# Kernel tuning notes

Measured on AMD Instinct MI355X. Metric: run time of the kernel, lower is better.

The kernel has to match this reference:

```python
import jax, jax.numpy as jnp
import numpy as np

N_LAYERS, HEADS, D_IN, D_OUT, T, D, DFF = 4, 8, 16, 3, 1024, 512, 2048
D_HEAD = D // HEADS


def sinusoidal_pos_enc(t, d):
    # Faithful to the source: base = pos / 10000**(emb_idx/d); sin on even cols, cos on odd cols
    pos = jnp.arange(t, dtype=jnp.float32)[:, None]
    emb = jnp.arange(d, dtype=jnp.float32)[None, :]
    base = pos / jnp.power(10000.0, emb / d)
    even = (jnp.arange(d) % 2 == 0)[None, :]
    return jnp.where(even, jnp.sin(base), jnp.cos(base))  # (t, d)


def layer_norm(x, g, b, eps=1e-5):
    m = x.mean(-1, keepdims=True)
    v = ((x - m) ** 2).mean(-1, keepdims=True)
    return (x - m) / jnp.sqrt(v + eps) * g + b


def setup_inputs() -> dict:
    key = jax.random.key(0)
    ks = iter(jax.random.split(key, 24))
    s = 0.02
    inp = {}
    inp['x'] = jax.random.normal(next(ks), (16, T, D_IN), dtype=jnp.float32)
    inp['pad_mask'] = jax.random.randint(next(ks), (16, T), 0, 2, dtype=jnp.int32)
    inp['enc_W'] = jax.random.normal(next(ks), (D_IN, D), dtype=jnp.float32) * s
    inp['enc_b'] = jnp.zeros((D,), jnp.float32)
    for name in ['Wq', 'Wk', 'Wv', 'Wo']:
        inp[name] = jax.random.normal(next(ks), (N_LAYERS, D, D), dtype=jnp.float32) * s
    inp['ff_W1'] = jax.random.normal(next(ks), (N_LAYERS, D, DFF), dtype=jnp.float32) * s
    inp['ff_b1'] = jnp.zeros((N_LAYERS, DFF), jnp.float32)
    inp['ff_W2'] = jax.random.normal(next(ks), (N_LAYERS, DFF, D), dtype=jnp.float32) * s
    inp['ff_b2'] = jnp.zeros((N_LAYERS, D), jnp.float32)
    inp['ln1_g'] = jnp.ones((N_LAYERS, D), jnp.float32)
    inp['ln1_b'] = jnp.zeros((N_LAYERS, D), jnp.float32)
    inp['ln2_g'] = jnp.ones((N_LAYERS, D), jnp.float32)
    inp['ln2_b'] = jnp.zeros((N_LAYERS, D), jnp.float32)
    inp['out_W'] = jax.random.normal(next(ks), (D * T, D_OUT), dtype=jnp.float32) * s
    inp['out_b'] = jnp.zeros((D_OUT,), jnp.float32)
    return inp


def reference(x, enc_W, enc_b, Wq, Wk, Wv, Wo, ff_W1, ff_b1, ff_W2, ff_b2,
              ln1_g, ln1_b, ln2_g, ln2_b, out_W, out_b, pad_mask):
    n, t = x.shape[0], x.shape[1]
    # InputEncoding (linear) scaled by sqrt(d_model)
    h = (x @ enc_W + enc_b) * jnp.sqrt(jnp.float32(D))
    # Sinusoidal positional encoding, zeroed at masked (pad_mask==0) timesteps
    pe = sinusoidal_pos_enc(t, D)[None]  # (1, t, d)
    pe = jnp.where(pad_mask[..., None] == 0, 0.0, pe)  # (n, t, d)
    h = h + pe
    mask4 = (pad_mask[..., None, None] == 0)  # (n, t, 1, 1)
    for i in range(N_LAYERS):
        # --- MultiHeadAttention (faithful to source's transpose quirk) ---
        Qh = (h @ Wq[i]).reshape(n, t, HEADS, D_HEAD).swapaxes(2, 3)  # (n,t,dh,H)
        Kh = (h @ Wk[i]).reshape(n, t, HEADS, D_HEAD)                 # (n,t,H,dh)
        Vh = (h @ Wv[i]).reshape(n, t, HEADS, D_HEAD).swapaxes(2, 3)  # (n,t,dh,H)
        # energy: per-timestep (dh x dh), scaled by d_head**1/2 == d_head/2 (source precedence)
        energy = jnp.matmul(Qh, Kh) / (D_HEAD / 2.0)                  # (n,t,dh,dh)
        energy = jnp.where(mask4, -1e20, energy)
        attn = jax.nn.softmax(energy, axis=-1)
        head = jnp.matmul(attn, Vh)                                   # (n,t,dh,H)
        out = head.reshape(n, t, D) @ Wo[i]
        # residual + layer norm
        h = layer_norm(out + h, ln1_g[i], ln1_b[i])
        # --- FFN (relu) ---
        ff = jax.nn.relu(h @ ff_W1[i] + ff_b1[i]) @ ff_W2[i] + ff_b2[i]
        h = layer_norm(ff + h, ln2_g[i], ln2_b[i])
    # mode='train': flatten and project
    return h.reshape(n, -1) @ out_W + out_b  # (n, d_output)
```

## Files before the change

### kernel.cpp

```cpp
#include <hip/hip_runtime.h>
#include <cmath>

#define NB 16
#define TSEQ 1024
#define DIN 16
#define DM 512
#define DFFN 2048
#define NLAYERS 4
#define DOUTN 3
#define ROWS (NB*TSEQ)

typedef unsigned short u16;
typedef unsigned int   u32;
typedef short bf16x8 __attribute__((ext_vector_type(8)));
typedef u16   u16x4  __attribute__((ext_vector_type(4)));
typedef float f32x4  __attribute__((ext_vector_type(4)));

__device__ __forceinline__ float b2f(u16 v) { return __uint_as_float((unsigned)v << 16); }
__device__ __forceinline__ u16 f2b(float f) {
    unsigned u = __float_as_uint(f);
    return (u16)((u + 0x7FFFu + ((u >> 16) & 1u)) >> 16);
}

#define GLL(gp, lp) __builtin_amdgcn_global_load_lds( \
    (const __attribute__((address_space(1))) unsigned int*)(gp), \
    (__attribute__((address_space(3))) unsigned int*)(lp), 16, 0, 0)

template<int PERM>
__global__ __launch_bounds__(256) void transpose_cast(
    const float* __restrict__ in, u16* __restrict__ out,
    int K, int N, size_t in_lstride, size_t out_lstride)
{
    in  += (size_t)blockIdx.z * in_lstride;
    out += (size_t)blockIdx.z * out_lstride;
    __shared__ float t[32][33];
    int bk = blockIdx.x * 32, bn = blockIdx.y * 32;
    int x = threadIdx.x & 31, y = threadIdx.x >> 5;
    #pragma unroll
    for (int i = 0; i < 32; i += 8)
        t[y + i][x] = in[(size_t)(bk + y + i) * N + bn + x];
    __syncthreads();
    #pragma unroll
    for (int i = 0; i < 32; i += 8) {
        int row = bn + y + i;
        if (PERM) row = ((row & 63) << 3) | ((row >> 6) & 7);
        out[(size_t)row * K + bk + x] = f2b(t[x][y + i]);
    }
}

__global__ __launch_bounds__(128) void pe_table_kernel(float* __restrict__ pe)
{
    int t = blockIdx.x;
    int c = threadIdx.x * 4;
    f32x4 o;
    #pragma unroll
    for (int j = 0; j < 4; ++j) {
        int d = c + j;
        float base = (float)t * powf(10000.0f, -(float)d * (1.0f/512.0f));
        o[j] = ((d & 1) == 0) ? sinf(base) : cosf(base);
    }
    *(f32x4*)&pe[(size_t)t * DM + c] = o;
}

__global__ __launch_bounds__(128) void encode_kernel(
    const float* __restrict__ x, const int* __restrict__ pad,
    const float* __restrict__ W, const float* __restrict__ b,
    const float* __restrict__ pe, u16* __restrict__ h)
{
    int row = blockIdx.x;
    int t   = row & (TSEQ - 1);
    int c   = threadIdx.x * 4;
    float acc[4];
    #pragma unroll
    for (int j = 0; j < 4; ++j) acc[j] = b[c + j];
    const float* xr = x + (size_t)row * DIN;
    #pragma unroll
    for (int k = 0; k < DIN; ++k) {
        float xv = xr[k];
        const float* wr = W + (size_t)k * DM + c;
        #pragma unroll
        for (int j = 0; j < 4; ++j) acc[j] += xv * wr[j];
    }
    const float s = 22.62741699796952f;
    bool has_pe = (pad[row] != 0);
    f32x4 pv = *(const f32x4*)&pe[(size_t)t * DM + c];
    u16x4 o;
    #pragma unroll
    for (int j = 0; j < 4; ++j) {
        acc[j] *= s;
        if (has_pe) acc[j] += pv[j];
        o[j] = f2b(acc[j]);
    }
    *(u16x4*)&h[(size_t)row * DM + c] = o;
}

template<int BIAS, int RELU>
__global__ __launch_bounds__(512, 4) void gemm_bf16(
    const u16* __restrict__ A, const u16* __restrict__ Bt,
    const float* __restrict__ bias, u16* __restrict__ C,
    int M, int N, int K)
{
    __shared__ u16 S[4][8192];
    const int tid  = threadIdx.x;
    const int lane = tid & 63;
    const int wid  = tid >> 6;
    const int wr   = wid >> 2;
    const int wc   = wid & 3;

    const int NY  = N >> 7;
    const int nwg = gridDim.x;
    const int cpx = nwg >> 3;
    const int bid = blockIdx.x;
    const int swz = (bid & 7) * cpx + (bid >> 3);
    const int bm  = (swz / NY) * 128;
    const int bn  = (swz % NY) * 128;

    const int srow8 = lane >> 3;
    const int sslot = lane & 7;
    const int scol  = ((sslot ^ srow8) * 8);
    const u16* Ag = A  + (size_t)(bm + wid * 16 + srow8) * K + scol;
    const u16* Bg = Bt + (size_t)(bn + wid * 16 + srow8) * K + scol;

    f32x4 acc[4][2];
    #pragma unroll
    for (int m = 0; m < 4; ++m)
        #pragma unroll
        for (int n = 0; n < 2; ++n)
            acc[m][n] = (f32x4){0.f, 0.f, 0.f, 0.f};

    const int fr  = lane & 15;
    const int grp = lane >> 4;

    auto STAGE = [&](int k0, int d) {
        u16* Al = S[d * 2 + 0] + wid * 1024;
        u16* Bl = S[d * 2 + 1] + wid * 1024;
        #pragma unroll
        for (int i = 0; i < 2; ++i) {
            GLL(Ag + (size_t)(i * 8) * K + k0, Al + i * 512);
            GLL(Bg + (size_t)(i * 8) * K + k0, Bl + i * 512);
        }
    };

    STAGE(0, 0);
    __syncthreads();

    int cur = 0;
    for (int k0 = 0; k0 < K; k0 += 64) {
        if (k0 + 64 < K) STAGE(k0 + 64, cur ^ 1);
        const u16* As = S[cur * 2 + 0];
        const u16* Bs = S[cur * 2 + 1];
        bf16x8 a[4][2];
        #pragma unroll
        for (int m = 0; m < 4; ++m) {
            int row = wr * 64 + m * 16 + fr;
            #pragma unroll
            for (int ks = 0; ks < 2; ++ks) {
                int slot = (ks * 4 + grp) ^ (row & 7);
                a[m][ks] = *(const bf16x8*)(As + row * 64 + slot * 8);
            }
        }
        #pragma unroll
        for (int n = 0; n < 2; ++n) {
            bf16x8 b[2];
            int row = wc * 32 + n * 16 + fr;
            #pragma unroll
            for (int ks = 0; ks < 2; ++ks) {
                int slot = (ks * 4 + grp) ^ (row & 7);
                b[ks] = *(const bf16x8*)(Bs + row * 64 + slot * 8);
            }
            #pragma unroll
            for (int m = 0; m < 4; ++m) {
                acc[m][n] = __builtin_amdgcn_mfma_f32_16x16x32_bf16(a[m][0], b[0], acc[m][n], 0, 0, 0);
                acc[m][n] = __builtin_amdgcn_mfma_f32_16x16x32_bf16(a[m][1], b[1], acc[m][n], 0, 0, 0);
            }
        }
        __syncthreads();
        cur ^= 1;
    }

    float bb[2] = {0.f, 0.f};
    if (BIAS) {
        #pragma unroll
        for (int n = 0; n < 2; ++n) bb[n] = bias[bn + wc * 32 + n * 16 + fr];
    }
    u16* Cs = (u16*)S;
    #pragma unroll
    for (int m = 0; m < 4; ++m)
        #pragma unroll
        for (int n = 0; n < 2; ++n)
            #pragma unroll
            for (int j = 0; j < 4; ++j) {
                int r = wr * 64 + m * 16 + grp * 4 + j;
                int c = wc * 32 + n * 16 + fr;
                float v = acc[m][n][j];
                if (BIAS) v += bb[n];
                if (RELU) v = fmaxf(v, 0.f);
                Cs[r * 136 + c] = f2b(v);
            }
    __syncthreads();
    #pragma unroll
    for (int p = 0; p < 4; ++p) {
        int r = p * 32 + (tid >> 4);
        int c = (tid & 15) * 8;
        bf16x8 v = *(const bf16x8*)(Cs + r * 136 + c);
        *(bf16x8*)(C + (size_t)(bm + r) * N + bn + c) = v;
    }
}

__global__ __launch_bounds__(256) void attn_mfma(
    const u16* __restrict__ QKV, const int* __restrict__ pad,
    u16* __restrict__ O)
{
    constexpr int WLDS = 2560;
    __shared__ u16 sh[4 * WLDS];
    const int wid  = threadIdx.x >> 6;
    const int lane = threadIdx.x & 63;
    const int site = blockIdx.x * 4 + wid;
    u16* P2 = sh + wid * WLDS;
    u16* Ol = P2 + 2048;

    const u16* base = QKV + (size_t)site * 1536;
    const int fr  = lane & 15;
    const int grp = lane >> 4;
    const bf16x8 zb = {0,0,0,0,0,0,0,0};
    const f32x4  zf = {0.f,0.f,0.f,0.f};

    if (pad[site] == 0) {
        bf16x8 vv = *(const bf16x8*)(base + 1024 + lane * 8);
        float s = 0.f;
        #pragma unroll
        for (int j = 0; j < 8; ++j) s += b2f((u16)vv[j]);
        s += __shfl_xor(s, 1); s += __shfl_xor(s, 2); s += __shfl_xor(s, 4);
        s *= (1.0f / 64.0f);
        bf16x8 ov;
        #pragma unroll
        for (int h2 = 0; h2 < 8; ++h2) ov[h2] = (short)f2b(__shfl(s, h2 * 8));
        *(bf16x8*)(O + (size_t)site * DM + lane * 8) = ov;
        return;
    }

    bf16x8 kt[4];
    #pragma unroll
    for (int n = 0; n < 4; ++n)
        kt[n] = (grp == 0) ? *(const bf16x8*)(base + 512 + (n * 16 + fr) * 8) : zb;
    bf16x8 bv[2];
    #pragma unroll
    for (int ks = 0; ks < 2; ++ks)
        bv[ks] = (fr < 8) ? *(const bf16x8*)(base + 1024 + fr * 64 + ks * 32 + grp * 8) : zb;

    const int swz = (fr & 3) ^ (fr >> 2);
    u16x4 pk23[4][2];

    #pragma unroll
    for (int m = 0; m < 4; ++m) {
        bf16x8 aq = (grp == 0) ? *(const bf16x8*)(base + (m * 16 + fr) * 8) : zb;
        f32x4 ev[4];
        #pragma unroll
        for (int n = 0; n < 4; ++n)
            ev[n] = __builtin_amdgcn_mfma_f32_16x16x32_bf16(kt[n], aq, zf, 0, 0, 0);
        f32x4 t0, t1;
        #pragma unroll
        for (int j = 0; j < 4; ++j) { t0[j] = fmaxf(ev[0][j], ev[1][j]); t1[j] = fmaxf(ev[2][j], ev[3][j]); }
        float mx = -1e30f;
        #pragma unroll
        for (int j = 0; j < 4; ++j) mx = fmaxf(mx, fmaxf(t0[j], t1[j]));
        mx = fmaxf(mx, __shfl_xor(mx, 16));
        mx = fmaxf(mx, __shfl_xor(mx, 32));
        float p[4][4];
        float s = 0.f;
        #pragma unroll
        for (int n = 0; n < 4; ++n)
            #pragma unroll
            for (int j = 0; j < 4; ++j) {
                p[n][j] = __expf((ev[n][j] - mx) * 0.03125f);
                s += p[n][j];
            }
        s += __shfl_xor(s, 16);
        s += __shfl_xor(s, 32);
        float inv = 1.0f / s;
        u16x4 pk[4];
        #pragma unroll
        for (int n = 0; n < 4; ++n)
            #pragma unroll
            for (int j = 0; j < 4; ++j) pk[n][j] = f2b(p[n][j] * inv);
        int row = m * 16 + fr;
        #pragma unroll
        for (int n = 0; n < 2; ++n) {
            int chunk = (n * 2 + (grp >> 1)) ^ swz;
            *(u16x4*)(P2 + row * 32 + chunk * 8 + (grp & 1) * 4) = pk[n];
        }
        pk23[m][0] = pk[2];
        pk23[m][1] = pk[3];
    }

    f32x4 pv[4];
    #pragma unroll
    for (int m = 0; m < 4; ++m) {
        int row = m * 16 + fr;
        bf16x8 ap = *(const bf16x8*)(P2 + row * 32 + ((grp ^ swz) * 8));
        pv[m] = __builtin_amdgcn_mfma_f32_16x16x32_bf16(ap, bv[0], zf, 0, 0, 0);
    }
    asm volatile("s_waitcnt lgkmcnt(0)" ::: "memory");
    __builtin_amdgcn_sched_barrier(0);

    #pragma unroll
    for (int m = 0; m < 4; ++m) {
        int row = m * 16 + fr;
        #pragma unroll
        for (int n = 0; n < 2; ++n) {
            int chunk = (n * 2 + (grp >> 1)) ^ swz;
            *(u16x4*)(P2 + row * 32 + chunk * 8 + (grp & 1) * 4) = pk23[m][n];
        }
    }
    #pragma unroll
    for (int m = 0; m < 4; ++m) {
        int row = m * 16 + fr;
        bf16x8 ap = *(const bf16x8*)(P2 + row * 32 + ((grp ^ swz) * 8));
        pv[m] = __builtin_amdgcn_mfma_f32_16x16x32_bf16(ap, bv[1], pv[m], 0, 0, 0);
    }

    #pragma unroll
    for (int m = 0; m < 4; ++m)
        #pragma unroll
        for (int j = 0; j < 4; ++j) {
            int row = m * 16 + grp * 4 + j;
            if (fr < 8) Ol[row * 8 + fr] = f2b(pv[m][j]);
        }
    bf16x8 o = *(const bf16x8*)(Ol + lane * 8);
    *(bf16x8*)(O + (size_t)site * DM + lane * 8) = o;
}

__global__ __launch_bounds__(256) void add_ln_kernel(
    const u16* __restrict__ A, u16* __restrict__ H,
    const float* __restrict__ g, const float* __restrict__ b)
{
    int row  = blockIdx.x * 4 + (threadIdx.x >> 6);
    int lane = threadIdx.x & 63;
    const u16* a = A + (size_t)row * DM + lane * 8;
    u16* h = H + (size_t)row * DM + lane * 8;
    bf16x8 av = *(const bf16x8*)a;
    bf16x8 hv = *(const bf16x8*)h;
    float v[8];
    float s = 0.f;
    #pragma unroll
    for (int j = 0; j < 8; ++j) { v[j] = b2f((u16)av[j]) + b2f((u16)hv[j]); s += v[j]; }
    #pragma unroll
    for (int off = 32; off > 0; off >>= 1) s += __shfl_xor(s, off, 64);
    float mean = s * (1.0f / 512.0f);
    float var = 0.f;
    #pragma unroll
    for (int j = 0; j < 8; ++j) { float d = v[j] - mean; var += d * d; }
    #pragma unroll
    for (int off = 32; off > 0; off >>= 1) var += __shfl_xor(var, off, 64);
    float rstd = rsqrtf(var * (1.0f / 512.0f) + 1e-5f);
    bf16x8 ov;
    #pragma unroll
    for (int j = 0; j < 8; ++j) {
        int d = lane * 8 + j;
        ov[j] = (short)f2b((v[j] - mean) * rstd * g[d] + b[d]);
    }
    *(bf16x8*)h = ov;
}

__global__ __launch_bounds__(256) void out_stage1(
    const u16* __restrict__ h, const float* __restrict__ W,
    float* __restrict__ partial)
{
    int b = blockIdx.x, s = blockIdx.y;
    int tid = threadIdx.x;
    const u16* hb = h + (size_t)b * (TSEQ * DM) + (size_t)s * 8192;
    const float* Wb = W + (size_t)s * 8192 * 3;
    float a0 = 0.f, a1 = 0.f, a2 = 0.f;
    #pragma unroll 4
    for (int it = 0; it < 32; ++it) {
        int i = it * 256 + tid;
        float hv = b2f(hb[i]);
        a0 += hv * Wb[i * 3 + 0];
        a1 += hv * Wb[i * 3 + 1];
        a2 += hv * Wb[i * 3 + 2];
    }
    __shared__ float red[3][256];
    red[0][tid] = a0; red[1][tid] = a1; red[2][tid] = a2;
    __syncthreads();
    for (int off = 128; off > 0; off >>= 1) {
        if (tid < off) {
            red[0][tid] += red[0][tid + off];
            red[1][tid] += red[1][tid + off];
            red[2][tid] += red[2][tid + off];
        }
        __syncthreads();
    }
    if (tid == 0) {
        partial[(b * 64 + s) * 3 + 0] = red[0][0];
        partial[(b * 64 + s) * 3 + 1] = red[1][0];
        partial[(b * 64 + s) * 3 + 2] = red[2][0];
    }
}

__global__ __launch_bounds__(64) void out_stage2(
    const float* __restrict__ partial, const float* __restrict__ ob,
    float* __restrict__ out)
{
    int t = threadIdx.x;
    if (t < NB * DOUTN) {
        int b = t / 3, o = t % 3;
        float s = ob[o];
        for (int k = 0; k < 64; ++k) s += partial[(b * 64 + k) * 3 + o];
        out[t] = s;
    }
}

extern "C" void kernel_launch(void* const* d_in, const int* in_sizes, int n_in,
                              void* d_out, int out_size, void* d_ws, size_t ws_size,
                              hipStream_t stream)
{
    const float* x    = (const float*)d_in[0];
    const int*   pad  = (const int*)  d_in[1];
    const float* encW = (const float*)d_in[2];
    const float* encB = (const float*)d_in[3];
    const float* Wq   = (const float*)d_in[4];
    const float* Wk   = (const float*)d_in[5];
    const float* Wv   = (const float*)d_in[6];
    const float* Wo   = (const float*)d_in[7];
    const float* fW1  = (const float*)d_in[8];
    const float* fb1  = (const float*)d_in[9];
    const float* fW2  = (const float*)d_in[10];
    const float* fb2  = (const float*)d_in[11];
    const float* l1g  = (const float*)d_in[12];
    const float* l1b  = (const float*)d_in[13];
    const float* l2g  = (const float*)d_in[14];
    const float* l2b  = (const float*)d_in[15];
    const float* outW = (const float*)d_in[16];
    const float* outB = (const float*)d_in[17];
    float* out = (float*)d_out;

    const size_t WL  = 3145728;
    const size_t BUF = (size_t)ROWS * DM;
    const size_t need = (4 * WL + 6 * BUF) * sizeof(u16) + (size_t)TSEQ * DM * sizeof(float);
    if (ws_size < need) return;
    u16* wt = (u16*)d_ws;
    u16* h  = wt + 4 * WL;
    u16* b0 = h  + BUF;
    u16* b3 = b0 + 3 * BUF;
    u16* b4 = b3 + BUF;
    float* pe = (float*)(b4 + BUF);

    transpose_cast<1><<<dim3(16,16,4), 256, 0, stream>>>(Wq,  wt + 0,       512,  512,  (size_t)512*512,  WL);
    transpose_cast<1><<<dim3(16,16,4), 256, 0, stream>>>(Wk,  wt + 262144,  512,  512,  (size_t)512*512,  WL);
    transpose_cast<0><<<dim3(16,16,4), 256, 0, stream>>>(Wv,  wt + 524288,  512,  512,  (size_t)512*512,  WL);
    transpose_cast<0><<<dim3(16,16,4), 256, 0, stream>>>(Wo,  wt + 786432,  512,  512,  (size_t)512*512,  WL);
    transpose_cast<0><<<dim3(16,64,4), 256, 0, stream>>>(fW1, wt + 1048576, 512,  2048, (size_t)512*2048, WL);
    transpose_cast<0><<<dim3(64,16,4), 256, 0, stream>>>(fW2, wt + 2097152, 2048, 512,  (size_t)2048*512, WL);

    pe_table_kernel<<<TSEQ, 128, 0, stream>>>(pe);
    encode_kernel<<<ROWS, 128, 0, stream>>>(x, pad, encW, encB, pe, h);

    for (int l = 0; l < NLAYERS; ++l) {
        u16* wl = wt + (size_t)l * WL;
        gemm_bf16<0,0><<<dim3((ROWS/128)*(1536/128)), 512, 0, stream>>>(h, wl, nullptr, b0, ROWS, 1536, DM);
        attn_mfma<<<ROWS/4, 256, 0, stream>>>(b0, pad, b3);
        gemm_bf16<0,0><<<dim3((ROWS/128)*(DM/128)), 512, 0, stream>>>(b3, wl + 786432, nullptr, b4, ROWS, DM, DM);
        add_ln_kernel<<<ROWS/4, 256, 0, stream>>>(b4, h, l1g + l*DM, l1b + l*DM);
        gemm_bf16<1,1><<<dim3((ROWS/128)*(DFFN/128)), 512, 0, stream>>>(h, wl + 1048576, fb1 + (size_t)l*DFFN, b0, ROWS, DFFN, DM);
        gemm_bf16<1,0><<<dim3((ROWS/128)*(DM/128)), 512, 0, stream>>>(b0, wl + 2097152, fb2 + (size_t)l*DM, b4, ROWS, DM, DFFN);
        add_ln_kernel<<<ROWS/4, 256, 0, stream>>>(b4, h, l2g + l*DM, l2b + l*DM);
    }

    out_stage1<<<dim3(NB, 64), 256, 0, stream>>>(h, outW, (float*)b0);
    out_stage2<<<1, 64, 0, stream>>>((float*)b0, outB, out);
}
```

Before: 727.3 us.

## Fuse residual add and LayerNorm into full-row GEMM epilogue for Wo and FFN2

```diff
diff --git a/kernel.cpp b/kernel.cpp
--- a/kernel.cpp
+++ b/kernel.cpp
@@ -207,6 +207,140 @@
     }
 }
 
+template<int BIAS>
+__global__ __launch_bounds__(512, 4) void gemm_ln(
+    const u16* __restrict__ A, const u16* __restrict__ Bt,
+    const float* __restrict__ bias, u16* __restrict__ H,
+    const float* __restrict__ g, const float* __restrict__ b, int K)
+{
+    __shared__ u16 S[2][17408];
+    const int tid  = threadIdx.x;
+    const int lane = tid & 63;
+    const int wid  = tid >> 6;
+
+    const int nwg = gridDim.x;
+    const int cpx = nwg >> 3;
+    const int bid = blockIdx.x;
+    const int swz = (bid & 7) * cpx + (bid >> 3);
+    const int bm  = swz * 32;
+
+    const int arow = (wid & 1) * 16 + (lane >> 2);
+    const int achk = (lane & 3) ^ ((arow >> 1) & 3);
+    const u16* Ag = A + (size_t)(bm + arow) * K + achk * 8;
+    const u16* Bg[4];
+    #pragma unroll
+    for (int j = 0; j < 4; ++j) {
+        int rB = wid * 64 + j * 16 + (lane >> 2);
+        int bchk = (lane & 3) ^ ((rB >> 1) & 3);
+        Bg[j] = Bt + (size_t)rB * K + bchk * 8;
+    }
+
+    f32x4 acc[2][4];
+    #pragma unroll
+    for (int m = 0; m < 2; ++m)
+        #pragma unroll
+        for (int n = 0; n < 4; ++n)
+            acc[m][n] = (f32x4){0.f, 0.f, 0.f, 0.f};
+
+    const int fr  = lane & 15;
+    const int grp = lane >> 4;
+
+    auto STAGE = [&](int k0, int d) {
+        if (wid < 2) GLL(Ag + k0, &S[d][0] + (wid * 64 + lane) * 8);
+        #pragma unroll
+        for (int j = 0; j < 4; ++j)
+            GLL(Bg[j] + k0, &S[d][1024] + ((wid * 4 + j) * 64 + lane) * 8);
+    };
+
+    STAGE(0, 0);
+    __syncthreads();
+
+    int cur = 0;
+    for (int k0 = 0; k0 < K; k0 += 32) {
+        if (k0 + 32 < K) STAGE(k0 + 32, cur ^ 1);
+        const u16* As = &S[cur][0];
+        const u16* Bs = &S[cur][1024];
+        bf16x8 a[2], bfr[4];
+        #pragma unroll
+        for (int m = 0; m < 2; ++m) {
+            int row = m * 16 + fr;
+            int slot = grp ^ ((row >> 1) & 3);
+            a[m] = *(const bf16x8*)(As + row * 32 + slot * 8);
+        }
+        #pragma unroll
+        for (int n = 0; n < 4; ++n) {
+            int row = wid * 64 + n * 16 + fr;
+            int slot = grp ^ ((row >> 1) & 3);
+            bfr[n] = *(const bf16x8*)(Bs + row * 32 + slot * 8);
+        }
+        #pragma unroll
+        for (int n = 0; n < 4; ++n)
+            #pragma unroll
+            for (int m = 0; m < 2; ++m)
+                acc[m][n] = __builtin_amdgcn_mfma_f32_16x16x32_bf16(a[m], bfr[n], acc[m][n], 0, 0, 0);
+        __syncthreads();
+        cur ^= 1;
+    }
+
+    float bb[4] = {0.f, 0.f, 0.f, 0.f};
+    if (BIAS) {
+        #pragma unroll
+        for (int n = 0; n < 4; ++n) bb[n] = bias[wid * 64 + n * 16 + fr];
+    }
+    u16* Cs = &S[0][0];
+    float* gl = (float*)(Cs + 16704);
+    float* bl = gl + 512;
+    #pragma unroll
+    for (int m = 0; m < 2; ++m)
+        #pragma unroll
+        for (int n = 0; n < 4; ++n)
+            #pragma unroll
+            for (int j = 0; j < 4; ++j) {
+                int r = m * 16 + grp * 4 + j;
+                int c = wid * 64 + n * 16 + fr;
+                Cs[r * 520 + c] = f2b(acc[m][n][j] + bb[n]);
+            }
+    gl[tid] = g[tid];
+    bl[tid] = b[tid];
+    __syncthreads();
+
+    int r  = wid * 4 + (lane >> 4);
+    int c0 = (lane & 15) * 32;
+    const u16* cr = Cs + r * 520 + c0;
+    u16* hr = H + (size_t)(bm + r) * DM + c0;
+    float v[32];
+    float s = 0.f;
+    #pragma unroll
+    for (int q = 0; q < 4; ++q) {
+        bf16x8 cv = *(const bf16x8*)(cr + q * 8);
+        bf16x8 hv = *(const bf16x8*)(hr + q * 8);
+        #pragma unroll
+        for (int j = 0; j < 8; ++j) {
+            v[q * 8 + j] = b2f((u16)cv[j]) + b2f((u16)hv[j]);
+            s += v[q * 8 + j];
+        }
+    }
+    s += __shfl_xor(s, 1); s += __shfl_xor(s, 2);
+    s += __shfl_xor(s, 4); s += __shfl_xor(s, 8);
+    float mean = s * (1.0f / 512.0f);
+    float var = 0.f;
+    #pragma unroll
+    for (int q = 0; q < 32; ++q) { float d = v[q] - mean; var += d * d; }
+    var += __shfl_xor(var, 1); var += __shfl_xor(var, 2);
+    var += __shfl_xor(var, 4); var += __shfl_xor(var, 8);
+    float rstd = rsqrtf(var * (1.0f / 512.0f) + 1e-5f);
+    #pragma unroll
+    for (int q = 0; q < 4; ++q) {
+        bf16x8 ov;
+        #pragma unroll
+        for (int j = 0; j < 8; ++j) {
+            int d = c0 + q * 8 + j;
+            ov[j] = (short)f2b((v[q * 8 + j] - mean) * rstd * gl[d] + bl[d]);
+        }
+        *(bf16x8*)(hr + q * 8) = ov;
+    }
+}
+
 __global__ __launch_bounds__(256) void attn_mfma(
     const u16* __restrict__ QKV, const int* __restrict__ pad,
     u16* __restrict__ O)
@@ -328,38 +462,6 @@
         }
     bf16x8 o = *(const bf16x8*)(Ol + lane * 8);
     *(bf16x8*)(O + (size_t)site * DM + lane * 8) = o;
-}
-
-__global__ __launch_bounds__(256) void add_ln_kernel(
-    const u16* __restrict__ A, u16* __restrict__ H,
-    const float* __restrict__ g, const float* __restrict__ b)
-{
-    int row  = blockIdx.x * 4 + (threadIdx.x >> 6);
-    int lane = threadIdx.x & 63;
-    const u16* a = A + (size_t)row * DM + lane * 8;
-    u16* h = H + (size_t)row * DM + lane * 8;
-    bf16x8 av = *(const bf16x8*)a;
-    bf16x8 hv = *(const bf16x8*)h;
-    float v[8];
-    float s = 0.f;
-    #pragma unroll
-    for (int j = 0; j < 8; ++j) { v[j] = b2f((u16)av[j]) + b2f((u16)hv[j]); s += v[j]; }
-    #pragma unroll
-    for (int off = 32; off > 0; off >>= 1) s += __shfl_xor(s, off, 64);
-    float mean = s * (1.0f / 512.0f);
-    float var = 0.f;
-    #pragma unroll
-    for (int j = 0; j < 8; ++j) { float d = v[j] - mean; var += d * d; }
-    #pragma unroll
-    for (int off = 32; off > 0; off >>= 1) var += __shfl_xor(var, off, 64);
-    float rstd = rsqrtf(var * (1.0f / 512.0f) + 1e-5f);
-    bf16x8 ov;
-    #pragma unroll
-    for (int j = 0; j < 8; ++j) {
-        int d = lane * 8 + j;
-        ov[j] = (short)f2b((v[j] - mean) * rstd * g[d] + b[d]);
-    }
-    *(bf16x8*)h = ov;
 }
 
 __global__ __launch_bounds__(256) void out_stage1(
@@ -459,11 +561,9 @@
         u16* wl = wt + (size_t)l * WL;
         gemm_bf16<0,0><<<dim3((ROWS/128)*(1536/128)), 512, 0, stream>>>(h, wl, nullptr, b0, ROWS, 1536, DM);
         attn_mfma<<<ROWS/4, 256, 0, stream>>>(b0, pad, b3);
-        gemm_bf16<0,0><<<dim3((ROWS/128)*(DM/128)), 512, 0, stream>>>(b3, wl + 786432, nullptr, b4, ROWS, DM, DM);
-        add_ln_kernel<<<ROWS/4, 256, 0, stream>>>(b4, h, l1g + l*DM, l1b + l*DM);
+        gemm_ln<0><<<ROWS/32, 512, 0, stream>>>(b3, wl + 786432, nullptr, h, l1g + l*DM, l1b + l*DM, DM);
         gemm_bf16<1,1><<<dim3((ROWS/128)*(DFFN/128)), 512, 0, stream>>>(h, wl + 1048576, fb1 + (size_t)l*DFFN, b0, ROWS, DFFN, DM);
-        gemm_bf16<1,0><<<dim3((ROWS/128)*(DM/128)), 512, 0, stream>>>(b0, wl + 2097152, fb2 + (size_t)l*DM, b4, ROWS, DM, DFFN);
-        add_ln_kernel<<<ROWS/4, 256, 0, stream>>>(b4, h, l2g + l*DM, l2b + l*DM);
+        gemm_ln<1><<<ROWS/32, 512, 0, stream>>>(b0, wl + 2097152, fb2 + (size_t)l*DM, h, l2g + l*DM, l2b + l*DM, DFFN);
     }
 
     out_stage1<<<dim3(NB, 64), 256, 0, stream>>>(h, outW, (float*)b0);
```

After: 890.4 us. 1.22x slower.
